# Kernel tuning notes

Measured on AMD Instinct MI355X. Metric: run time of the kernel, lower is better.

The kernel has to match this reference:

```python
import jax, jax.numpy as jnp
import numpy as np

N_NODES = 50000
N_EDGES = 200000
IN_FEATS = 32
OUT_FEATS = 32
EDGE_DIM = 16


def setup_inputs() -> dict:
    key = jax.random.key(0)
    k1, k2, k3, k4, k5 = jax.random.split(key, 5)
    feat = jax.random.normal(k1, (N_NODES, IN_FEATS), dtype=jnp.float32)
    efeat = jax.random.normal(k2, (N_EDGES, EDGE_DIM), dtype=jnp.float32)
    src = jax.random.randint(k3, (N_EDGES,), 0, N_NODES, dtype=jnp.int32)
    dst = jax.random.randint(k4, (N_EDGES,), 0, N_NODES, dtype=jnp.int32)
    # edge_func = Linear(EDGE_DIM -> IN_FEATS*OUT_FEATS)
    W_edge = jax.random.normal(k5, (EDGE_DIM, IN_FEATS * OUT_FEATS), dtype=jnp.float32) * (1.0 / np.sqrt(EDGE_DIM))
    b_edge = jnp.zeros((IN_FEATS * OUT_FEATS,), dtype=jnp.float32)
    bias = jnp.zeros((OUT_FEATS,), dtype=jnp.float32)
    return {"feat": feat, "efeat": efeat, "src": src, "dst": dst,
            "W_edge": W_edge, "b_edge": b_edge, "bias": bias}


def reference(feat, efeat, src, dst, W_edge, b_edge, bias):
    # edge_func: (E, edge_dim) -> (E, in, out) edge-conditioned weights
    w = (efeat @ W_edge + b_edge).reshape(-1, IN_FEATS, OUT_FEATS)
    # u_mul_e + sum over in dim  ==  per-edge matvec: h_src[e] @ W[e]
    h_src = feat[src]                               # (E, in) gather
    msg = jnp.einsum('ei,eio->eo', h_src, w)        # (E, out)
    # mean reduce over incoming edges per destination node
    agg = jax.ops.segment_sum(msg, dst, num_segments=N_NODES)   # (N, out)
    deg = jax.ops.segment_sum(jnp.ones((msg.shape[0],), dtype=msg.dtype), dst,
                              num_segments=N_NODES)
    agg = agg / jnp.maximum(deg, 1.0)[:, None]      # zero-degree nodes stay 0
    return agg + bias
```

## Files before the change

kernel.cpp:

```cpp
#include <hip/hip_runtime.h>
#include <hip/hip_bf16.h>

#define NNODES 50000
#define NEDGES 200000
#define WCT_ROW 552
#define WCT_BYTES (32 * WCT_ROW * 2)
#define HROW 40
#define TILE_EDGES 64
#define NTILES (NEDGES / TILE_EDGES)
#define CHAIN_BLKS ((NEDGES + 255) / 256)
#define DROW 36

#define MSG_OFF   0
#define HEAD_OFF  25600000
#define NEXT_OFF  25800000
#define WCT_OFF   26600000

using f32x4 = __attribute__((ext_vector_type(4))) float;
using f16x2 = __attribute__((ext_vector_type(2))) _Float16;
using f16x4 = __attribute__((ext_vector_type(4))) _Float16;
using f16x8 = __attribute__((ext_vector_type(8))) _Float16;

__device__ __forceinline__ f16x2 pkrtz(float a, float b) {
    return __builtin_bit_cast(f16x2, __builtin_amdgcn_cvt_pkrtz(a, b));
}

__device__ __forceinline__ void gload_lds16(const void* g, void* l) {
    __builtin_amdgcn_global_load_lds(
        (const __attribute__((address_space(1))) unsigned int*)g,
        (__attribute__((address_space(3))) unsigned int*)l, 16, 0, 0);
}

#define WCT_BLKS 69
__global__ void init_kernel(const float* __restrict__ W_edge,
                            const float* __restrict__ b_edge,
                            _Float16* __restrict__ wct,
                            unsigned* __restrict__ head) {
    int b = blockIdx.x;
    if (b < WCT_BLKS) {
        int gid = b * 256 + threadIdx.x;
        if (gid >= 32 * WCT_ROW) return;
        int n = gid / WCT_ROW;
        int c = gid - n * WCT_ROW;
        float v = 0.0f;
        if (c < 512)      v = W_edge[(c & 15) * 1024 + (c >> 4) * 32 + n];
        else if (c < 544) v = b_edge[(c - 512) * 32 + n];
        wct[gid] = (_Float16)v;
    } else {
        int gid = (b - WCT_BLKS) * 256 + threadIdx.x;
        if (gid < NNODES) head[gid] = 0xFFFFFFFFu;
    }
}

__global__ __launch_bounds__(256, 3) void work_kernel(
    const float* __restrict__ feat, const float* __restrict__ efeat,
    const int* __restrict__ src, const int* __restrict__ dst,
    const _Float16* __restrict__ wct_g,
    float* __restrict__ msg, unsigned* __restrict__ head,
    unsigned* __restrict__ next) {

    __shared__ __align__(16) unsigned short wct_lds[32 * WCT_ROW];
    __shared__ __align__(16) unsigned short h_lds[TILE_EDGES * HROW];
    __shared__ __align__(16) float dtile[TILE_EDGES * DROW];

    const int t = threadIdx.x;

    if (blockIdx.x >= NTILES) {
        int e = (blockIdx.x - NTILES) * 256 + t;
        if (e < NEDGES)
            next[e] = atomicExch(&head[dst[e]], (unsigned)e);
        return;
    }

    const int lane = t & 63;
    const int wave = t >> 6;
    const int ebase = blockIdx.x * TILE_EDGES;

    {
        const char* gsrc = (const char*)wct_g;
        char* lbase = (char*)wct_lds;
        #pragma unroll
        for (int c = 0; c < 9; ++c) {
            int chunk = wave + c * 4;
            if (chunk < 35) {
                int boff = (chunk << 10) + lane * 16;
                if (boff < WCT_BYTES) gload_lds16(gsrc + boff, lbase + boff);
            }
        }
    }

    {
        int et = t >> 2, p = t & 3;
        int se = src[ebase + et];
        const float* fp = feat + se * 32 + p * 8;
        float4 a = *(const float4*)fp;
        float4 b = *(const float4*)(fp + 4);
        uint4 hp;
        hp.x = __builtin_bit_cast(unsigned int, pkrtz(a.x, a.y));
        hp.y = __builtin_bit_cast(unsigned int, pkrtz(a.z, a.w));
        hp.z = __builtin_bit_cast(unsigned int, pkrtz(b.x, b.y));
        hp.w = __builtin_bit_cast(unsigned int, pkrtz(b.z, b.w));
        *(uint4*)(void*)(h_lds + et * HROW + p * 8) = hp;
    }

    const int r16 = lane & 15;
    const int g   = lane >> 4;
    const int wbase = wave * 16;
    const int eg = ebase + wbase + r16;

    const float* efp = efeat + eg * 16 + (g & 1) * 8;
    float4 e0 = *(const float4*)efp;
    float4 e1 = *(const float4*)(efp + 4);
    f16x2 ef2[4] = { pkrtz(e0.x, e0.y), pkrtz(e0.z, e0.w),
                     pkrtz(e1.x, e1.y), pkrtz(e1.z, e1.w) };

    __syncthreads();

    unsigned int hbc[16];
    {
        const uint4* hrow = (const uint4*)(void*)(h_lds + (wbase + r16) * HROW);
        unsigned int hw[16];
        #pragma unroll
        for (int q = 0; q < 4; ++q) {
            uint4 v = hrow[q];
            hw[q*4+0] = v.x; hw[q*4+1] = v.y; hw[q*4+2] = v.z; hw[q*4+3] = v.w;
        }
        const bool hi = (g >> 1) & 1;
        #pragma unroll
        for (int s = 0; s < 16; ++s) {
            unsigned int x = hi ? (hw[s] >> 16) : (hw[s] & 0xffffu);
            hbc[s] = x | (x << 16);
        }
    }

    const _Float16* brow0 = (const _Float16*)wct_lds + r16 * WCT_ROW;
    const _Float16* brow1 = (const _Float16*)wct_lds + (16 + r16) * WCT_ROW;

    f32x4 acc0 = {0.f, 0.f, 0.f, 0.f};
    f32x4 acc1 = {0.f, 0.f, 0.f, 0.f};

    #pragma unroll
    for (int s = 0; s < 16; ++s) {
        const int koff = s * 32 + g * 8;
        f16x8 b0 = *(const f16x8*)(brow0 + koff);
        f16x8 b1 = *(const f16x8*)(brow1 + koff);
        f16x2 hb = __builtin_bit_cast(f16x2, hbc[s]);
        f16x2 p0 = hb * ef2[0], p1 = hb * ef2[1], p2 = hb * ef2[2], p3 = hb * ef2[3];
        f16x4 lo  = __builtin_shufflevector(p0, p1, 0, 1, 2, 3);
        f16x4 hi4 = __builtin_shufflevector(p2, p3, 0, 1, 2, 3);
        f16x8 af  = __builtin_shufflevector(lo, hi4, 0, 1, 2, 3, 4, 5, 6, 7);
        acc0 = __builtin_amdgcn_mfma_f32_16x16x32_f16(af, b0, acc0, 0, 0, 0);
        acc1 = __builtin_amdgcn_mfma_f32_16x16x32_f16(af, b1, acc1, 0, 0, 0);
    }
    {
        const int koff = 512 + g * 8;
        f16x8 b0 = *(const f16x8*)(brow0 + koff);
        f16x8 b1 = *(const f16x8*)(brow1 + koff);
        f16x8 af = *(const f16x8*)(void*)((const _Float16*)h_lds + (wbase + r16) * HROW + g * 8);
        acc0 = __builtin_amdgcn_mfma_f32_16x16x32_f16(af, b0, acc0, 0, 0, 0);
        acc1 = __builtin_amdgcn_mfma_f32_16x16x32_f16(af, b1, acc1, 0, 0, 0);
    }

    {
        const int browD = wbase + g * 4;
        #pragma unroll
        for (int r = 0; r < 4; ++r) {
            dtile[(browD + r) * DROW + r16]      = acc0[r];
            dtile[(browD + r) * DROW + 16 + r16] = acc1[r];
        }
    }
    __syncthreads();

    {
        const int et = t >> 2, q = t & 3;
        const float* drow = dtile + et * DROW + q * 8;
        float4 v0 = *(const float4*)(drow);
        float4 v1 = *(const float4*)(drow + 4);
        float* mp = msg + (ebase + et) * 32 + q * 8;
        *(float4*)(mp)     = v0;
        *(float4*)(mp + 4) = v1;
    }
}

__global__ __launch_bounds__(256) void pull_kernel(
    const float* __restrict__ msg, const unsigned* __restrict__ head,
    const unsigned* __restrict__ next, const float* __restrict__ bias,
    float* __restrict__ out) {

    int n = blockIdx.x * 256 + threadIdx.x;
    if (n >= NNODES) return;

    float4 s0 = {0,0,0,0}, s1 = {0,0,0,0}, s2 = {0,0,0,0}, s3 = {0,0,0,0};
    float4 s4 = {0,0,0,0}, s5 = {0,0,0,0}, s6 = {0,0,0,0}, s7 = {0,0,0,0};
    float degf = 0.0f;

    unsigned e = head[n];
    while (e != 0xFFFFFFFFu) {
        const float4* mp = (const float4*)(msg + e * 32);
        float4 m0 = mp[0], m1 = mp[1], m2 = mp[2], m3 = mp[3];
        float4 m4 = mp[4], m5 = mp[5], m6 = mp[6], m7 = mp[7];
        s0.x+=m0.x; s0.y+=m0.y; s0.z+=m0.z; s0.w+=m0.w;
        s1.x+=m1.x; s1.y+=m1.y; s1.z+=m1.z; s1.w+=m1.w;
        s2.x+=m2.x; s2.y+=m2.y; s2.z+=m2.z; s2.w+=m2.w;
        s3.x+=m3.x; s3.y+=m3.y; s3.z+=m3.z; s3.w+=m3.w;
        s4.x+=m4.x; s4.y+=m4.y; s4.z+=m4.z; s4.w+=m4.w;
        s5.x+=m5.x; s5.y+=m5.y; s5.z+=m5.z; s5.w+=m5.w;
        s6.x+=m6.x; s6.y+=m6.y; s6.z+=m6.z; s6.w+=m6.w;
        s7.x+=m7.x; s7.y+=m7.y; s7.z+=m7.z; s7.w+=m7.w;
        degf += 1.0f;
        e = next[e];
    }

    float inv = 1.0f / fmaxf(degf, 1.0f);
    const float4* bp = (const float4*)bias;
    float4 o;
    float* op = out + n * 32;
    #define EMIT(S, Q) \
        o.x = S.x*inv + bp[Q].x; o.y = S.y*inv + bp[Q].y; \
        o.z = S.z*inv + bp[Q].z; o.w = S.w*inv + bp[Q].w; \
        *(float4*)(op + Q*4) = o;
    EMIT(s0,0) EMIT(s1,1) EMIT(s2,2) EMIT(s3,3)
    EMIT(s4,4) EMIT(s5,5) EMIT(s6,6) EMIT(s7,7)
    #undef EMIT
}

extern "C" void kernel_launch(void* const* d_in, const int* in_sizes, int n_in,
                              void* d_out, int out_size, void* d_ws, size_t ws_size,
                              hipStream_t stream) {
    const float* feat   = (const float*)d_in[0];
    const float* efeat  = (const float*)d_in[1];
    const int*   src    = (const int*)d_in[2];
    const int*   dst    = (const int*)d_in[3];
    const float* W_edge = (const float*)d_in[4];
    const float* b_edge = (const float*)d_in[5];
    const float* bias   = (const float*)d_in[6];

    char* ws = (char*)d_ws;
    float*    msg  = (float*)(ws + MSG_OFF);
    unsigned* head = (unsigned*)(ws + HEAD_OFF);
    unsigned* next = (unsigned*)(ws + NEXT_OFF);
    _Float16* wct  = (_Float16*)(ws + WCT_OFF);
    float*    out  = (float*)d_out;

    init_kernel<<<WCT_BLKS + (NNODES + 255) / 256, 256, 0, stream>>>(
        W_edge, b_edge, wct, head);
    work_kernel<<<NTILES + CHAIN_BLKS, 256, 0, stream>>>(
        feat, efeat, src, dst, wct, msg, head, next);
    pull_kernel<<<(NNODES + 255) / 256, 256, 0, stream>>>(
        msg, head, next, bias, out);
}
```

Measured before the change: 48.21 us.

## Make work kernel persistent, gather features per lane, split pull across lanes

The work kernel becomes persistent with 768 blocks looping over edge tiles. Each block stages the edge-weight table into LDS once instead of once per tile. Each lane now gathers its source feature row straight from global memory into registers, which removes the h_lds staging buffer and its barrier; the linked-list atomics are folded into the tile loop. The pull kernel gives each node to 8 threads, one float4 column chunk each, for more parallelism and coalesced message reads, at the cost of every one of those threads walking the same linked list.

```diff
diff --git a/kernel.cpp b/kernel.cpp
--- a/kernel.cpp
+++ b/kernel.cpp
@@ -5,10 +5,9 @@
 #define NEDGES 200000
 #define WCT_ROW 552
 #define WCT_BYTES (32 * WCT_ROW * 2)
-#define HROW 40
 #define TILE_EDGES 64
 #define NTILES (NEDGES / TILE_EDGES)
-#define CHAIN_BLKS ((NEDGES + 255) / 256)
+#define WORK_BLOCKS 768
 #define DROW 36
 
 #define MSG_OFF   0
@@ -60,21 +59,14 @@
     unsigned* __restrict__ next) {
 
     __shared__ __align__(16) unsigned short wct_lds[32 * WCT_ROW];
-    __shared__ __align__(16) unsigned short h_lds[TILE_EDGES * HROW];
     __shared__ __align__(16) float dtile[TILE_EDGES * DROW];
 
     const int t = threadIdx.x;
-
-    if (blockIdx.x >= NTILES) {
-        int e = (blockIdx.x - NTILES) * 256 + t;
-        if (e < NEDGES)
-            next[e] = atomicExch(&head[dst[e]], (unsigned)e);
-        return;
-    }
-
     const int lane = t & 63;
     const int wave = t >> 6;
-    const int ebase = blockIdx.x * TILE_EDGES;
+    const int r16 = lane & 15;
+    const int g   = lane >> 4;
+    const int wbase = wave * 16;
 
     {
         const char* gsrc = (const char*)wct_g;
@@ -88,97 +80,102 @@
             }
         }
     }
-
-    {
-        int et = t >> 2, p = t & 3;
-        int se = src[ebase + et];
-        const float* fp = feat + se * 32 + p * 8;
-        float4 a = *(const float4*)fp;
-        float4 b = *(const float4*)(fp + 4);
-        uint4 hp;
-        hp.x = __builtin_bit_cast(unsigned int, pkrtz(a.x, a.y));
-        hp.y = __builtin_bit_cast(unsigned int, pkrtz(a.z, a.w));
-        hp.z = __builtin_bit_cast(unsigned int, pkrtz(b.x, b.y));
-        hp.w = __builtin_bit_cast(unsigned int, pkrtz(b.z, b.w));
-        *(uint4*)(void*)(h_lds + et * HROW + p * 8) = hp;
-    }
-
-    const int r16 = lane & 15;
-    const int g   = lane >> 4;
-    const int wbase = wave * 16;
-    const int eg = ebase + wbase + r16;
-
-    const float* efp = efeat + eg * 16 + (g & 1) * 8;
-    float4 e0 = *(const float4*)efp;
-    float4 e1 = *(const float4*)(efp + 4);
-    f16x2 ef2[4] = { pkrtz(e0.x, e0.y), pkrtz(e0.z, e0.w),
-                     pkrtz(e1.x, e1.y), pkrtz(e1.z, e1.w) };
-
     __syncthreads();
 
-    unsigned int hbc[16];
-    {
-        const uint4* hrow = (const uint4*)(void*)(h_lds + (wbase + r16) * HROW);
-        unsigned int hw[16];
-        #pragma unroll
-        for (int q = 0; q < 4; ++q) {
-            uint4 v = hrow[q];
-            hw[q*4+0] = v.x; hw[q*4+1] = v.y; hw[q*4+2] = v.z; hw[q*4+3] = v.w;
-        }
-        const bool hi = (g >> 1) & 1;
+    const _Float16* brow0 = (const _Float16*)wct_lds + r16 * WCT_ROW;
+    const _Float16* brow1 = (const _Float16*)wct_lds + (16 + r16) * WCT_ROW;
+
+    for (int tile = blockIdx.x; tile < NTILES; tile += WORK_BLOCKS) {
+        const int ebase = tile * TILE_EDGES;
+
+        if (t < TILE_EDGES) {
+            int e = ebase + t;
+            next[e] = atomicExch(&head[dst[e]], (unsigned)e);
+        }
+
+        const int eg = ebase + wbase + r16;
+
+        const float* efp = efeat + eg * 16 + (g & 1) * 8;
+        float4 e0 = *(const float4*)efp;
+        float4 e1 = *(const float4*)(efp + 4);
+        f16x2 ef2[4] = { pkrtz(e0.x, e0.y), pkrtz(e0.z, e0.w),
+                         pkrtz(e1.x, e1.y), pkrtz(e1.z, e1.w) };
+
+        unsigned hw[16];
+        {
+            const int se = src[eg];
+            const float4* fp = (const float4*)(feat + se * 32);
+            #pragma unroll
+            for (int q = 0; q < 8; ++q) {
+                float4 v = fp[q];
+                hw[2*q+0] = __builtin_bit_cast(unsigned, pkrtz(v.x, v.y));
+                hw[2*q+1] = __builtin_bit_cast(unsigned, pkrtz(v.z, v.w));
+            }
+        }
+
+        unsigned hbc[16];
+        {
+            const bool hi = (g >> 1) & 1;
+            #pragma unroll
+            for (int s = 0; s < 16; ++s) {
+                unsigned x = hi ? (hw[s] >> 16) : (hw[s] & 0xffffu);
+                hbc[s] = x | (x << 16);
+            }
+        }
+
+        f32x4 acc0 = {0.f, 0.f, 0.f, 0.f};
+        f32x4 acc1 = {0.f, 0.f, 0.f, 0.f};
+
         #pragma unroll
         for (int s = 0; s < 16; ++s) {
-            unsigned int x = hi ? (hw[s] >> 16) : (hw[s] & 0xffffu);
-            hbc[s] = x | (x << 16);
-        }
-    }
-
-    const _Float16* brow0 = (const _Float16*)wct_lds + r16 * WCT_ROW;
-    const _Float16* brow1 = (const _Float16*)wct_lds + (16 + r16) * WCT_ROW;
-
-    f32x4 acc0 = {0.f, 0.f, 0.f, 0.f};
-    f32x4 acc1 = {0.f, 0.f, 0.f, 0.f};
-
-    #pragma unroll
-    for (int s = 0; s < 16; ++s) {
-        const int koff = s * 32 + g * 8;
-        f16x8 b0 = *(const f16x8*)(brow0 + koff);
-        f16x8 b1 = *(const f16x8*)(brow1 + koff);
-        f16x2 hb = __builtin_bit_cast(f16x2, hbc[s]);
-        f16x2 p0 = hb * ef2[0], p1 = hb * ef2[1], p2 = hb * ef2[2], p3 = hb * ef2[3];
-        f16x4 lo  = __builtin_shufflevector(p0, p1, 0, 1, 2, 3);
-        f16x4 hi4 = __builtin_shufflevector(p2, p3, 0, 1, 2, 3);
-        f16x8 af  = __builtin_shufflevector(lo, hi4, 0, 1, 2, 3, 4, 5, 6, 7);
-        acc0 = __builtin_amdgcn_mfma_f32_16x16x32_f16(af, b0, acc0, 0, 0, 0);
-        acc1 = __builtin_amdgcn_mfma_f32_16x16x32_f16(af, b1, acc1, 0, 0, 0);
-    }
-    {
-        const int koff = 512 + g * 8;
-        f16x8 b0 = *(const f16x8*)(brow0 + koff);
-        f16x8 b1 = *(const f16x8*)(brow1 + koff);
-        f16x8 af = *(const f16x8*)(void*)((const _Float16*)h_lds + (wbase + r16) * HROW + g * 8);
-        acc0 = __builtin_amdgcn_mfma_f32_16x16x32_f16(af, b0, acc0, 0, 0, 0);
-        acc1 = __builtin_amdgcn_mfma_f32_16x16x32_f16(af, b1, acc1, 0, 0, 0);
-    }
-
-    {
-        const int browD = wbase + g * 4;
-        #pragma unroll
-        for (int r = 0; r < 4; ++r) {
-            dtile[(browD + r) * DROW + r16]      = acc0[r];
-            dtile[(browD + r) * DROW + 16 + r16] = acc1[r];
-        }
-    }
-    __syncthreads();
-
-    {
-        const int et = t >> 2, q = t & 3;
-        const float* drow = dtile + et * DROW + q * 8;
-        float4 v0 = *(const float4*)(drow);
-        float4 v1 = *(const float4*)(drow + 4);
-        float* mp = msg + (ebase + et) * 32 + q * 8;
-        *(float4*)(mp)     = v0;
-        *(float4*)(mp + 4) = v1;
+            const int koff = s * 32 + g * 8;
+            f16x8 b0 = *(const f16x8*)(brow0 + koff);
+            f16x8 b1 = *(const f16x8*)(brow1 + koff);
+            f16x2 hb = __builtin_bit_cast(f16x2, hbc[s]);
+            f16x2 p0 = hb * ef2[0], p1 = hb * ef2[1], p2 = hb * ef2[2], p3 = hb * ef2[3];
+            f16x4 lo  = __builtin_shufflevector(p0, p1, 0, 1, 2, 3);
+            f16x4 hi4 = __builtin_shufflevector(p2, p3, 0, 1, 2, 3);
+            f16x8 af  = __builtin_shufflevector(lo, hi4, 0, 1, 2, 3, 4, 5, 6, 7);
+            acc0 = __builtin_amdgcn_mfma_f32_16x16x32_f16(af, b0, acc0, 0, 0, 0);
+            acc1 = __builtin_amdgcn_mfma_f32_16x16x32_f16(af, b1, acc1, 0, 0, 0);
+        }
+        {
+            uint4 bwv;
+            unsigned* bw = (unsigned*)&bwv;
+            #pragma unroll
+            for (int j = 0; j < 4; ++j) {
+                unsigned lo2 = (g & 1) ? hw[4 + j]  : hw[j];
+                unsigned hi2 = (g & 1) ? hw[12 + j] : hw[8 + j];
+                bw[j] = (g & 2) ? hi2 : lo2;
+            }
+            f16x8 af = __builtin_bit_cast(f16x8, bwv);
+            const int koff = 512 + g * 8;
+            f16x8 b0 = *(const f16x8*)(brow0 + koff);
+            f16x8 b1 = *(const f16x8*)(brow1 + koff);
+            acc0 = __builtin_amdgcn_mfma_f32_16x16x32_f16(af, b0, acc0, 0, 0, 0);
+            acc1 = __builtin_amdgcn_mfma_f32_16x16x32_f16(af, b1, acc1, 0, 0, 0);
+        }
+
+        __syncthreads();
+        {
+            const int browD = wbase + g * 4;
+            #pragma unroll
+            for (int r = 0; r < 4; ++r) {
+                dtile[(browD + r) * DROW + r16]      = acc0[r];
+                dtile[(browD + r) * DROW + 16 + r16] = acc1[r];
+            }
+        }
+        __syncthreads();
+
+        {
+            const int et = t >> 2, q = t & 3;
+            const float* drow = dtile + et * DROW + q * 8;
+            float4 v0 = *(const float4*)(drow);
+            float4 v1 = *(const float4*)(drow + 4);
+            float* mp = msg + (ebase + et) * 32 + q * 8;
+            *(float4*)(mp)     = v0;
+            *(float4*)(mp + 4) = v1;
+        }
     }
 }
 
@@ -187,41 +184,25 @@
     const unsigned* __restrict__ next, const float* __restrict__ bias,
     float* __restrict__ out) {
 
-    int n = blockIdx.x * 256 + threadIdx.x;
-    if (n >= NNODES) return;
-
-    float4 s0 = {0,0,0,0}, s1 = {0,0,0,0}, s2 = {0,0,0,0}, s3 = {0,0,0,0};
-    float4 s4 = {0,0,0,0}, s5 = {0,0,0,0}, s6 = {0,0,0,0}, s7 = {0,0,0,0};
+    int gid = blockIdx.x * 256 + threadIdx.x;
+    if (gid >= NNODES * 8) return;
+    int n = gid >> 3, q = gid & 7;
+
+    float4 s = {0.f, 0.f, 0.f, 0.f};
     float degf = 0.0f;
 
     unsigned e = head[n];
     while (e != 0xFFFFFFFFu) {
-        const float4* mp = (const float4*)(msg + e * 32);
-        float4 m0 = mp[0], m1 = mp[1], m2 = mp[2], m3 = mp[3];
-        float4 m4 = mp[4], m5 = mp[5], m6 = mp[6], m7 = mp[7];
-        s0.x+=m0.x; s0.y+=m0.y; s0.z+=m0.z; s0.w+=m0.w;
-        s1.x+=m1.x; s1.y+=m1.y; s1.z+=m1.z; s1.w+=m1.w;
-        s2.x+=m2.x; s2.y+=m2.y; s2.z+=m2.z; s2.w+=m2.w;
-        s3.x+=m3.x; s3.y+=m3.y; s3.z+=m3.z; s3.w+=m3.w;
-        s4.x+=m4.x; s4.y+=m4.y; s4.z+=m4.z; s4.w+=m4.w;
-        s5.x+=m5.x; s5.y+=m5.y; s5.z+=m5.z; s5.w+=m5.w;
-        s6.x+=m6.x; s6.y+=m6.y; s6.z+=m6.z; s6.w+=m6.w;
-        s7.x+=m7.x; s7.y+=m7.y; s7.z+=m7.z; s7.w+=m7.w;
+        float4 m = *(const float4*)(msg + e * 32 + q * 4);
+        s.x += m.x; s.y += m.y; s.z += m.z; s.w += m.w;
         degf += 1.0f;
         e = next[e];
     }
 
     float inv = 1.0f / fmaxf(degf, 1.0f);
-    const float4* bp = (const float4*)bias;
-    float4 o;
-    float* op = out + n * 32;
-    #define EMIT(S, Q) \
-        o.x = S.x*inv + bp[Q].x; o.y = S.y*inv + bp[Q].y; \
-        o.z = S.z*inv + bp[Q].z; o.w = S.w*inv + bp[Q].w; \
-        *(float4*)(op + Q*4) = o;
-    EMIT(s0,0) EMIT(s1,1) EMIT(s2,2) EMIT(s3,3)
-    EMIT(s4,4) EMIT(s5,5) EMIT(s6,6) EMIT(s7,7)
-    #undef EMIT
+    float4 b = ((const float4*)bias)[q];
+    float4 o = { s.x * inv + b.x, s.y * inv + b.y, s.z * inv + b.z, s.w * inv + b.w };
+    *(float4*)(out + n * 32 + q * 4) = o;
 }
 
 extern "C" void kernel_launch(void* const* d_in, const int* in_sizes, int n_in,
@@ -244,8 +225,8 @@
 
     init_kernel<<<WCT_BLKS + (NNODES + 255) / 256, 256, 0, stream>>>(
         W_edge, b_edge, wct, head);
-    work_kernel<<<NTILES + CHAIN_BLKS, 256, 0, stream>>>(
+    work_kernel<<<WORK_BLOCKS, 256, 0, stream>>>(
         feat, efeat, src, dst, wct, msg, head, next);
-    pull_kernel<<<(NNODES + 255) / 256, 256, 0, stream>>>(
+    pull_kernel<<<(NNODES * 8 + 255) / 256, 256, 0, stream>>>(
         msg, head, next, bias, out);
 }
```

Result: slower. 59.87 us (+24.2%).

## Split pull reduction across 8 threads per node and re-layout msg stores

Applied to the files above, without the earlier changes.

The pull kernel now assigns 8 threads per destination node, each accumulating one float4 slice, instead of one thread reading all 32 floats per edge. This raises parallelism and memory-level concurrency in the latency-bound linked-list walk. The message buffer layout is changed so work_kernel writes fully contiguous per-block float4 stores, and pull indexes it with a matching permutation. The cost is that each of the 8 threads walks the same next[] chain redundantly. The bias-row A-fragment load is also hoisted earlier.

```diff
diff --git a/kernel.cpp b/kernel.cpp
--- a/kernel.cpp
+++ b/kernel.cpp
@@ -56,7 +56,7 @@
     const float* __restrict__ feat, const float* __restrict__ efeat,
     const int* __restrict__ src, const int* __restrict__ dst,
     const _Float16* __restrict__ wct_g,
-    float* __restrict__ msg, unsigned* __restrict__ head,
+    float4* __restrict__ msg4, unsigned* __restrict__ head,
     unsigned* __restrict__ next) {
 
     __shared__ __align__(16) unsigned short wct_lds[32 * WCT_ROW];
@@ -117,6 +117,7 @@
     __syncthreads();
 
     unsigned int hbc[16];
+    f16x8 af_bias;
     {
         const uint4* hrow = (const uint4*)(void*)(h_lds + (wbase + r16) * HROW);
         unsigned int hw[16];
@@ -131,6 +132,7 @@
             unsigned int x = hi ? (hw[s] >> 16) : (hw[s] & 0xffffu);
             hbc[s] = x | (x << 16);
         }
+        af_bias = *(const f16x8*)(void*)((const _Float16*)h_lds + (wbase + r16) * HROW + g * 8);
     }
 
     const _Float16* brow0 = (const _Float16*)wct_lds + r16 * WCT_ROW;
@@ -156,9 +158,8 @@
         const int koff = 512 + g * 8;
         f16x8 b0 = *(const f16x8*)(brow0 + koff);
         f16x8 b1 = *(const f16x8*)(brow1 + koff);
-        f16x8 af = *(const f16x8*)(void*)((const _Float16*)h_lds + (wbase + r16) * HROW + g * 8);
-        acc0 = __builtin_amdgcn_mfma_f32_16x16x32_f16(af, b0, acc0, 0, 0, 0);
-        acc1 = __builtin_amdgcn_mfma_f32_16x16x32_f16(af, b1, acc1, 0, 0, 0);
+        acc0 = __builtin_amdgcn_mfma_f32_16x16x32_f16(af_bias, b0, acc0, 0, 0, 0);
+        acc1 = __builtin_amdgcn_mfma_f32_16x16x32_f16(af_bias, b1, acc1, 0, 0, 0);
     }
 
     {
@@ -176,52 +177,38 @@
         const float* drow = dtile + et * DROW + q * 8;
         float4 v0 = *(const float4*)(drow);
         float4 v1 = *(const float4*)(drow + 4);
-        float* mp = msg + (ebase + et) * 32 + q * 8;
-        *(float4*)(mp)     = v0;
-        *(float4*)(mp + 4) = v1;
+        float4* mp = msg4 + (size_t)blockIdx.x * 512;
+        mp[t]       = v0;
+        mp[256 + t] = v1;
     }
 }
 
 __global__ __launch_bounds__(256) void pull_kernel(
-    const float* __restrict__ msg, const unsigned* __restrict__ head,
+    const float4* __restrict__ msg4, const unsigned* __restrict__ head,
     const unsigned* __restrict__ next, const float* __restrict__ bias,
     float* __restrict__ out) {
 
-    int n = blockIdx.x * 256 + threadIdx.x;
-    if (n >= NNODES) return;
-
-    float4 s0 = {0,0,0,0}, s1 = {0,0,0,0}, s2 = {0,0,0,0}, s3 = {0,0,0,0};
-    float4 s4 = {0,0,0,0}, s5 = {0,0,0,0}, s6 = {0,0,0,0}, s7 = {0,0,0,0};
+    int gid = blockIdx.x * 256 + threadIdx.x;
+    if (gid >= NNODES * 8) return;
+    int n = gid >> 3, Q = gid & 7;
+
+    const unsigned qoff = (unsigned)((Q & 1) * 256 + (Q >> 1));
+
+    float4 s = {0.f, 0.f, 0.f, 0.f};
     float degf = 0.0f;
 
     unsigned e = head[n];
     while (e != 0xFFFFFFFFu) {
-        const float4* mp = (const float4*)(msg + e * 32);
-        float4 m0 = mp[0], m1 = mp[1], m2 = mp[2], m3 = mp[3];
-        float4 m4 = mp[4], m5 = mp[5], m6 = mp[6], m7 = mp[7];
-        s0.x+=m0.x; s0.y+=m0.y; s0.z+=m0.z; s0.w+=m0.w;
-        s1.x+=m1.x; s1.y+=m1.y; s1.z+=m1.z; s1.w+=m1.w;
-        s2.x+=m2.x; s2.y+=m2.y; s2.z+=m2.z; s2.w+=m2.w;
-        s3.x+=m3.x; s3.y+=m3.y; s3.z+=m3.z; s3.w+=m3.w;
-        s4.x+=m4.x; s4.y+=m4.y; s4.z+=m4.z; s4.w+=m4.w;
-        s5.x+=m5.x; s5.y+=m5.y; s5.z+=m5.z; s5.w+=m5.w;
-        s6.x+=m6.x; s6.y+=m6.y; s6.z+=m6.z; s6.w+=m6.w;
-        s7.x+=m7.x; s7.y+=m7.y; s7.z+=m7.z; s7.w+=m7.w;
+        float4 m = msg4[(size_t)(e >> 6) * 512 + qoff + (e & 63) * 4];
+        s.x += m.x; s.y += m.y; s.z += m.z; s.w += m.w;
         degf += 1.0f;
         e = next[e];
     }
 
     float inv = 1.0f / fmaxf(degf, 1.0f);
-    const float4* bp = (const float4*)bias;
-    float4 o;
-    float* op = out + n * 32;
-    #define EMIT(S, Q) \
-        o.x = S.x*inv + bp[Q].x; o.y = S.y*inv + bp[Q].y; \
-        o.z = S.z*inv + bp[Q].z; o.w = S.w*inv + bp[Q].w; \
-        *(float4*)(op + Q*4) = o;
-    EMIT(s0,0) EMIT(s1,1) EMIT(s2,2) EMIT(s3,3)
-    EMIT(s4,4) EMIT(s5,5) EMIT(s6,6) EMIT(s7,7)
-    #undef EMIT
+    float4 b = ((const float4*)bias)[Q];
+    float4 o = { s.x * inv + b.x, s.y * inv + b.y, s.z * inv + b.z, s.w * inv + b.w };
+    *(float4*)(out + n * 32 + Q * 4) = o;
 }
 
 extern "C" void kernel_launch(void* const* d_in, const int* in_sizes, int n_in,
@@ -236,7 +223,7 @@
     const float* bias   = (const float*)d_in[6];
 
     char* ws = (char*)d_ws;
-    float*    msg  = (float*)(ws + MSG_OFF);
+    float4*   msg4 = (float4*)(ws + MSG_OFF);
     unsigned* head = (unsigned*)(ws + HEAD_OFF);
     unsigned* next = (unsigned*)(ws + NEXT_OFF);
     _Float16* wct  = (_Float16*)(ws + WCT_OFF);
@@ -245,7 +232,7 @@
     init_kernel<<<WCT_BLKS + (NNODES + 255) / 256, 256, 0, stream>>>(
         W_edge, b_edge, wct, head);
     work_kernel<<<NTILES + CHAIN_BLKS, 256, 0, stream>>>(
-        feat, efeat, src, dst, wct, msg, head, next);
-    pull_kernel<<<(NNODES + 255) / 256, 256, 0, stream>>>(
-        msg, head, next, bias, out);
-}
+        feat, efeat, src, dst, wct, msg4, head, next);
+    pull_kernel<<<(NNODES * 8 + 255) / 256, 256, 0, stream>>>(
+        msg4, head, next, bias, out);
+}
```

New measurement: 46.44 us. 1.04x faster.
